# Kernel optimization log

Hardware: AMD Instinct MI355X
Metric: run time of the kernel (lower is better)

Reference implementation:

```python
import jax, jax.numpy as jnp
import numpy as np

B, T, D = 32, 1024, 1024  # batch, t_k (encoder steps), attn_sz == cell_state_sz


def setup_inputs() -> dict:
    key = jax.random.key(0)
    ks = jax.random.split(key, 7)
    scale = 1.0 / np.sqrt(D)
    return {
        "h_i": jax.random.normal(ks[0], (B, T, D), jnp.float32),
        "s_t": jax.random.normal(ks[1], (B, D), jnp.float32),
        "coverage": jax.random.uniform(ks[2], (B, T), jnp.float32),
        "W_h": jax.random.normal(ks[3], (D, D), jnp.float32) * scale,
        "W_s": jax.random.normal(ks[4], (D, D), jnp.float32) * scale,
        "b_s": jnp.zeros((D,), jnp.float32),
        "W_c": jax.random.normal(ks[5], (D,), jnp.float32) * scale,  # Dense(1 -> D) kernel
        "V_w": jax.random.normal(ks[6], (D,), jnp.float32) * scale,  # Dense(D -> 1) kernel
    }


def reference(h_i, s_t, coverage, W_h, W_s, b_s, W_c, V_w):
    # enc_features = W_h(h_i): (B, T, D)
    enc_features = jnp.einsum("btd,de->bte", h_i, W_h)
    # dec_features = W_s(s_t) broadcast over time: (B, 1, D)
    dec_features = (s_t @ W_s + b_s)[:, None, :]
    # coverage features: scalar coverage per step times (1->D) kernel
    cov_features = coverage[:, :, None] * W_c[None, None, :]
    features = enc_features + dec_features + cov_features
    # e_t = V(tanh(features)) squeezed to (B, T)
    e_t = jnp.einsum("btd,d->bt", jnp.tanh(features), V_w)
    a_t = jax.nn.softmax(e_t, axis=1)
    coverage_new = coverage + a_t
    # context = a_t @ h_i : (B, D)
    context_vector = jnp.einsum("bt,btd->bd", a_t, h_i)
    return context_vector, a_t, coverage_new
```

## Files before the change

### kernel.cpp

```cpp
#include <hip/hip_runtime.h>

#define B_ 32
#define T_ 1024
#define D_ 1024
#define M_ (B_ * T_)
#define NT_ 8
#define NT2 4
#define BM_ 128
#define BN_ 128
#define BK_ 64
#define NKT (D_ / BK_)
#define LSTR 72

#define FENCE_ALL() asm volatile("s_waitcnt vmcnt(0) lgkmcnt(0)" ::: "memory")

typedef __attribute__((ext_vector_type(8))) short short8;
typedef __attribute__((ext_vector_type(4))) float f32x4;

__device__ __forceinline__ unsigned f2bf(float f) {
    union { float f; unsigned u; } v; v.f = f;
    return (v.u + 0x7FFFu + ((v.u >> 16) & 1u)) >> 16;
}
__device__ __forceinline__ unsigned pack2(float a, float b) {
    return f2bf(a) | (f2bf(b) << 16);
}
__device__ __forceinline__ float bf2f(unsigned hi16) {
    union { unsigned u; float f; } v; v.u = hi16 << 16;
    return v.f;
}
__device__ __forceinline__ float fast_tanh(float x) {
    x = fminf(15.0f, fmaxf(-15.0f, x));
    float e = __expf(2.0f * x);
    return (e - 1.0f) * __fdividef(1.0f, e + 1.0f);
}

#define PREP_CONVH_BLKS 2048
#define PREP_CONVWT_BLKS 256
#define PREP_DEC_BLKS (B_ * 16)
__global__ __launch_bounds__(256) void prep_kernel(
    const float* __restrict__ h_i, uint4* __restrict__ h_bf4,
    const float* __restrict__ W_h, unsigned short* __restrict__ Wt,
    const float* __restrict__ s_t, const float* __restrict__ W_s,
    const float* __restrict__ b_s, float* __restrict__ dec_part)
{
    __shared__ float smem[64 * 65];
    const int bid = blockIdx.x;
    const int tid = threadIdx.x;
    if (bid < PREP_CONVH_BLKS) {
        const int idx = bid * 256 + tid;
        const int stride = PREP_CONVH_BLKS * 256;
        const int ngroups = M_ * D_ / 8;
        const float4* in4 = (const float4*)h_i;
        for (int g = idx; g < ngroups; g += stride) {
            const float4 a = in4[2 * g];
            const float4 b = in4[2 * g + 1];
            h_bf4[g] = make_uint4(pack2(a.x, a.y), pack2(a.z, a.w),
                                  pack2(b.x, b.y), pack2(b.z, b.w));
        }
    } else if (bid < PREP_CONVH_BLKS + PREP_CONVWT_BLKS) {
        const int tb = bid - PREP_CONVH_BLKS;
        float (*tile)[65] = (float (*)[65])smem;
        const int k0 = (tb & 15) * 64;
        const int n0 = (tb >> 4) * 64;
        const int tx = tid & 63, ty = tid >> 6;
#pragma unroll
        for (int r = 0; r < 16; ++r) {
            const int row = ty * 16 + r;
            tile[row][tx] = W_h[(size_t)(k0 + row) * D_ + n0 + tx];
        }
        __syncthreads();
#pragma unroll
        for (int r = 0; r < 16; ++r) {
            const int row = ty * 16 + r;
            Wt[(size_t)(n0 + row) * D_ + k0 + tx] = (unsigned short)f2bf(tile[tx][row]);
        }
    } else {
        const int db = bid - (PREP_CONVH_BLKS + PREP_CONVWT_BLKS);
        const int kc = db & 3;
        const int nc = (db >> 2) & 3;
        const int b  = db >> 4;
        const int d = nc * 256 + tid;
        const int k0 = kc * 256;
        float* s_lds = smem;
        s_lds[tid] = s_t[b * D_ + k0 + tid];
        __syncthreads();
        float acc = (kc == 0) ? b_s[d] : 0.f;
#pragma unroll 8
        for (int k = 0; k < 256; ++k) acc += s_lds[k] * W_s[(size_t)(k0 + k) * D_ + d];
        dec_part[kc * (B_ * D_) + b * D_ + d] = acc;
    }
}

__global__ __launch_bounds__(512, 2) void attn_gemm2(
    const unsigned short* __restrict__ h_bf, const unsigned short* __restrict__ wt_bf,
    const float* __restrict__ dec_part, const float* __restrict__ coverage,
    const float* __restrict__ W_c, const float* __restrict__ V_w,
    float* __restrict__ e_part)
{
    __shared__ __align__(16) unsigned short lds2[2][2][256 * 64];
    __shared__ float e_red[4][256];

    const int tid = threadIdx.x;
    const int nt2 = blockIdx.x >> 7;
    const int mt  = blockIdx.x & 127;
    const int m0 = mt * 256;
    const int n0 = nt2 * 256;
    const int bb = m0 >> 10;

    const int wave = tid >> 6;
    const int lane = tid & 63;
    const int wr = wave >> 2;
    const int wc = wave & 3;
    const int lr = lane & 15;
    const int lk = lane >> 4;

    f32x4 acc[8][4];
    const f32x4 fzero = {0.f, 0.f, 0.f, 0.f};
#pragma unroll
    for (int i = 0; i < 8; ++i)
#pragma unroll
        for (int j = 0; j < 4; ++j) acc[i][j] = fzero;

    const char* gA = (const char*)h_bf + (size_t)m0 * (D_ * 2);
    const char* gB = (const char*)wt_bf + (size_t)n0 * (D_ * 2);
    const int lrow8 = lane >> 3;
    const int scol = (((lane & 7) ^ lrow8) << 4);
    const int sw = (lr & 7) << 4;

#define GLOAD(mat, chunk, kt, buf)                                                 \
    {                                                                              \
        const int row_ = (chunk) * 8 + lrow8;                                      \
        const size_t goff_ = (size_t)row_ * (D_ * 2) + (size_t)(kt) * 128 + scol;  \
        __builtin_amdgcn_global_load_lds(                                          \
            (const __attribute__((address_space(1))) void*)(((mat) ? gB : gA) + goff_), \
            (__attribute__((address_space(3))) void*)((char*)lds2 +                \
                ((buf) * 2 + (mat)) * 32768 + (chunk) * 1024), 16, 0, 0);          \
    }
#define ST_BLO(buf, kt) { GLOAD(1, 2 * wave, kt, buf); GLOAD(1, 2 * wave + 1, kt, buf); }
#define ST_BHI(buf, kt) { GLOAD(1, 16 + 2 * wave, kt, buf); GLOAD(1, 16 + 2 * wave + 1, kt, buf); }
#define ST_AU(buf, kt, g)                                                          \
    { const int c_ = (wave < 4) ? ((g) * 4 + wave) : (16 + (g) * 4 + (wave - 4));  \
      GLOAD(0, c_, kt, buf); }

#define PH_BAR(N)                                                                  \
    asm volatile("s_waitcnt vmcnt(" #N ")" ::: "memory");                          \
    __builtin_amdgcn_s_barrier();                                                  \
    asm volatile("" ::: "memory")

#define LOADA(g)                                                                   \
    _Pragma("unroll")                                                              \
    for (int m = 0; m < 2; ++m)                                                    \
        _Pragma("unroll")                                                          \
        for (int kk = 0; kk < 2; ++kk)                                             \
            aA[m][kk] = *(const short8*)(ldsA +                                    \
                (wr * 128 + ((g) * 2 + m) * 16 + lr) * 128 +                       \
                ((kk * 64 + lk * 16) ^ sw));

#define MFMAQ(g)                                                                   \
    __builtin_amdgcn_s_setprio(1);                                                 \
    _Pragma("unroll")                                                              \
    for (int m = 0; m < 2; ++m)                                                    \
        _Pragma("unroll")                                                          \
        for (int ni = 0; ni < 4; ++ni)                                             \
            _Pragma("unroll")                                                      \
            for (int kk = 0; kk < 2; ++kk)                                         \
                acc[(g) * 2 + m][ni] = __builtin_amdgcn_mfma_f32_16x16x32_bf16(    \
                    aA[m][kk], bB[ni][kk], acc[(g) * 2 + m][ni], 0, 0, 0);         \
    __builtin_amdgcn_s_setprio(0);

    ST_BLO(0, 0); ST_BHI(0, 0);
    ST_AU(0, 0, 0); ST_AU(0, 0, 1); ST_AU(0, 0, 2); ST_AU(0, 0, 3);
    FENCE_ALL();
    __syncthreads();

    for (int kt = 0; kt < NKT; ++kt) {
        const int cur = kt & 1;
        const int nxt = cur ^ 1;
        const int ktn = (kt + 1) & (NKT - 1);
        const char* ldsA = (const char*)lds2 + (cur * 2 + 0) * 32768;
        const char* ldsB = (const char*)lds2 + (cur * 2 + 1) * 32768;

        short8 aA[2][2];
        short8 bB[4][2];

        PH_BAR(3);
#pragma unroll
        for (int ni = 0; ni < 4; ++ni)
#pragma unroll
            for (int kk = 0; kk < 2; ++kk)
                bB[ni][kk] = *(const short8*)(ldsB +
                    (wc * 64 + ni * 16 + lr) * 128 + ((kk * 64 + lk * 16) ^ sw));
        LOADA(0);
        ST_BLO(nxt, ktn);
        MFMAQ(0);

        PH_BAR(4);
        LOADA(1);
        ST_BHI(nxt, ktn);
        ST_AU(nxt, ktn, 0);
        MFMAQ(1);

        PH_BAR(5);
        LOADA(2);
        ST_AU(nxt, ktn, 1);
        ST_AU(nxt, ktn, 2);
        MFMAQ(2);

        PH_BAR(7);
        LOADA(3);
        ST_AU(nxt, ktn, 3);
        MFMAQ(3);
    }
#undef GLOAD
#undef ST_BLO
#undef ST_BHI
#undef ST_AU
#undef PH_BAR
#undef LOADA
#undef MFMAQ

    FENCE_ALL();
    __syncthreads();

    float esum[8][4];
    float covv[8][4];
#pragma unroll
    for (int mi = 0; mi < 8; ++mi)
#pragma unroll
        for (int r = 0; r < 4; ++r) {
            esum[mi][r] = 0.f;
            covv[mi][r] = coverage[m0 + wr * 128 + mi * 16 + lk * 4 + r];
        }
    const float* dp = dec_part + bb * D_;
#pragma unroll
    for (int ni = 0; ni < 4; ++ni) {
        const int n = n0 + wc * 64 + ni * 16 + lr;
        const float vw = V_w[n];
        const float dc = dp[n] + dp[B_ * D_ + n] + dp[2 * B_ * D_ + n] + dp[3 * B_ * D_ + n];
        const float wcv = W_c[n];
#pragma unroll
        for (int mi = 0; mi < 8; ++mi)
#pragma unroll
            for (int r = 0; r < 4; ++r) {
                const float f = acc[mi][ni][r] + dc + covv[mi][r] * wcv;
                esum[mi][r] += fast_tanh(f) * vw;
            }
    }
#pragma unroll
    for (int off = 1; off <= 8; off <<= 1)
#pragma unroll
        for (int mi = 0; mi < 8; ++mi)
#pragma unroll
            for (int r = 0; r < 4; ++r)
                esum[mi][r] += __shfl_xor(esum[mi][r], off, 64);

    if (lr == 0) {
#pragma unroll
        for (int mi = 0; mi < 8; ++mi)
#pragma unroll
            for (int r = 0; r < 4; ++r)
                e_red[wc][wr * 128 + mi * 16 + lk * 4 + r] = esum[mi][r];
    }
    FENCE_ALL();
    __syncthreads();
    if (tid < 256)
        e_part[(size_t)nt2 * M_ + m0 + tid] =
            e_red[0][tid] + e_red[1][tid] + e_red[2][tid] + e_red[3][tid];
}

__global__ __launch_bounds__(256, 2) void attn_gemm_kernel(
    const float* __restrict__ h_i, const float* __restrict__ W_h,
    const float* __restrict__ dec_part, const float* __restrict__ coverage,
    const float* __restrict__ W_c, const float* __restrict__ V_w,
    float* __restrict__ e_part)
{
    __shared__ __align__(16) unsigned short lA[BM_][LSTR];
    __shared__ __align__(16) unsigned short lB[BN_][LSTR];
    __shared__ float e_red[256];

    const int tid = threadIdx.x;
    const int nt = blockIdx.x >> 8;
    const int mt = blockIdx.x & 255;
    const int m0 = mt * BM_;
    const int n0 = nt * BN_;
    const int bb = m0 >> 10;

    const int wave = tid >> 6;
    const int lane = tid & 63;
    const int wr = wave >> 1, wc = wave & 1;
    const int lr = lane & 15;
    const int lk = lane >> 4;

    f32x4 acc[4][4];
    const f32x4 fzero = {0.f, 0.f, 0.f, 0.f};
#pragma unroll
    for (int i = 0; i < 4; ++i)
#pragma unroll
        for (int j = 0; j < 4; ++j) acc[i][j] = fzero;

    const int a_row = tid >> 4;
    const int a_k = (tid & 15) << 2;
    const float* hA = h_i + (size_t)m0 * D_;

    for (int k0 = 0; k0 < D_; k0 += BK_) {
#pragma unroll
        for (int p = 0; p < 8; ++p) {
            const int row = a_row + p * 16;
            const float4 v = *(const float4*)(hA + (size_t)row * D_ + (k0 + a_k));
            *(uint2*)&lA[row][a_k] = make_uint2(pack2(v.x, v.y), pack2(v.z, v.w));
        }
#pragma unroll
        for (int p = 0; p < 8; ++p) {
            const int task = tid + p * 256;
            const int n = task & 127;
            const int kg = task >> 7;
            const float* wp = W_h + (size_t)(k0 + kg * 4) * D_ + n0 + n;
            const float x0 = wp[0 * D_], x1 = wp[1 * D_], x2 = wp[2 * D_], x3 = wp[3 * D_];
            *(uint2*)&lB[n][kg * 4] = make_uint2(pack2(x0, x1), pack2(x2, x3));
        }
        __syncthreads();

        short8 af[2][4], bfr[2][4];
#pragma unroll
        for (int kk = 0; kk < 2; ++kk)
#pragma unroll
            for (int i = 0; i < 4; ++i) {
                af[kk][i]  = *(const short8*)&lA[wr * 64 + i * 16 + lr][kk * 32 + lk * 8];
                bfr[kk][i] = *(const short8*)&lB[wc * 64 + i * 16 + lr][kk * 32 + lk * 8];
            }
#pragma unroll
        for (int kk = 0; kk < 2; ++kk)
#pragma unroll
            for (int mi = 0; mi < 4; ++mi)
#pragma unroll
                for (int ni = 0; ni < 4; ++ni)
                    acc[mi][ni] = __builtin_amdgcn_mfma_f32_16x16x32_bf16(
                        af[kk][mi], bfr[kk][ni], acc[mi][ni], 0, 0, 0);
        __syncthreads();
    }

    float esum[4][4];
    float covv[4][4];
#pragma unroll
    for (int mi = 0; mi < 4; ++mi)
#pragma unroll
        for (int r = 0; r < 4; ++r) {
            esum[mi][r] = 0.f;
            covv[mi][r] = coverage[m0 + wr * 64 + mi * 16 + lk * 4 + r];
        }
    const float* dp = dec_part + bb * D_;
#pragma unroll
    for (int ni = 0; ni < 4; ++ni) {
        const int n = n0 + wc * 64 + ni * 16 + lr;
        const float vw = V_w[n];
        const float dc = dp[n] + dp[B_ * D_ + n] + dp[2 * B_ * D_ + n] + dp[3 * B_ * D_ + n];
        const float wcv = W_c[n];
#pragma unroll
        for (int mi = 0; mi < 4; ++mi)
#pragma unroll
            for (int r = 0; r < 4; ++r) {
                const float f = acc[mi][ni][r] + dc + covv[mi][r] * wcv;
                esum[mi][r] += fast_tanh(f) * vw;
            }
    }
#pragma unroll
    for (int off = 1; off <= 8; off <<= 1)
#pragma unroll
        for (int mi = 0; mi < 4; ++mi)
#pragma unroll
            for (int r = 0; r < 4; ++r)
                esum[mi][r] += __shfl_xor(esum[mi][r], off, 64);

    if (lr == 0) {
#pragma unroll
        for (int mi = 0; mi < 4; ++mi)
#pragma unroll
            for (int r = 0; r < 4; ++r)
                e_red[wc * 128 + wr * 64 + mi * 16 + lk * 4 + r] = esum[mi][r];
    }
    __syncthreads();
    if (tid < 128)
        e_part[(size_t)nt * M_ + m0 + tid] = e_red[tid] + e_red[128 + tid];
}

__global__ __launch_bounds__(256) void softmax_kernel(
    const float* __restrict__ e_part, const float* __restrict__ coverage,
    float* __restrict__ a_out, float* __restrict__ cov_out,
    float* __restrict__ a_ws, int nparts)
{
    const int b = blockIdx.x;
    const int tid = threadIdx.x;
    __shared__ float redmx[4], redsum[4];
    float e[4];
#pragma unroll
    for (int j = 0; j < 4; ++j) {
        const int t = tid + j * 256;
        float s = 0.f;
        for (int p = 0; p < nparts; ++p) s += e_part[(size_t)p * M_ + b * T_ + t];
        e[j] = s;
    }
    float mx = fmaxf(fmaxf(e[0], e[1]), fmaxf(e[2], e[3]));
#pragma unroll
    for (int off = 32; off > 0; off >>= 1) mx = fmaxf(mx, __shfl_xor(mx, off, 64));
    if ((tid & 63) == 0) redmx[tid >> 6] = mx;
    __syncthreads();
    mx = fmaxf(fmaxf(redmx[0], redmx[1]), fmaxf(redmx[2], redmx[3]));
    float p4[4];
    float ps = 0.f;
#pragma unroll
    for (int j = 0; j < 4; ++j) { p4[j] = __expf(e[j] - mx); ps += p4[j]; }
#pragma unroll
    for (int off = 32; off > 0; off >>= 1) ps += __shfl_xor(ps, off, 64);
    if ((tid & 63) == 0) redsum[tid >> 6] = ps;
    __syncthreads();
    ps = redsum[0] + redsum[1] + redsum[2] + redsum[3];
    const float inv = __fdividef(1.f, ps);
#pragma unroll
    for (int j = 0; j < 4; ++j) {
        const int idx = b * T_ + tid + j * 256;
        const float a = p4[j] * inv;
        a_out[idx] = a;
        a_ws[idx] = a;
        cov_out[idx] = coverage[idx] + a;
    }
}

__global__ __launch_bounds__(256) void ctx_part_bf(
    const unsigned short* __restrict__ h_bf, const float* __restrict__ a_t,
    float* __restrict__ ctx_part)
{
    const int bid = blockIdx.x;
    const int b = bid >> 3;
    const int dc = (bid >> 2) & 1;
    const int tc = bid & 3;
    const int tid = threadIdx.x;
    const int d0 = dc * 512 + tid * 2;
    __shared__ float a_lds[256];
    a_lds[tid] = a_t[b * T_ + tc * 256 + tid];
    __syncthreads();
    const unsigned short* hp = h_bf + ((size_t)(b * T_ + tc * 256)) * D_ + d0;
    float acc0 = 0.f, acc1 = 0.f;
#pragma unroll 8
    for (int t = 0; t < 256; ++t) {
        const unsigned v = *(const unsigned*)(hp + (size_t)t * D_);
        const float a = a_lds[t];
        acc0 += a * bf2f(v & 0xFFFFu);
        acc1 += a * bf2f(v >> 16);
    }
    *(float2*)(ctx_part + tc * (B_ * D_) + b * D_ + d0) = make_float2(acc0, acc1);
}

__global__ __launch_bounds__(256) void ctx_part_f32(
    const float* __restrict__ h_i, const float* __restrict__ a_t,
    float* __restrict__ ctx_part)
{
    const int bid = blockIdx.x;
    const int b = bid >> 4;
    const int dc = (bid >> 2) & 3;
    const int tc = bid & 3;
    const int tid = threadIdx.x;
    const int d = dc * 256 + tid;
    __shared__ float a_lds[256];
    a_lds[tid] = a_t[b * T_ + tc * 256 + tid];
    __syncthreads();
    const float* hp = h_i + ((size_t)(b * T_ + tc * 256)) * D_ + d;
    float acc = 0.f;
#pragma unroll 8
    for (int t = 0; t < 256; ++t) acc += a_lds[t] * hp[(size_t)t * D_];
    ctx_part[tc * (B_ * D_) + b * D_ + d] = acc;
}

__global__ __launch_bounds__(256) void dec_kernel(
    const float* __restrict__ s_t, const float* __restrict__ W_s,
    const float* __restrict__ b_s, float* __restrict__ dec_part)
{
    const int bid = blockIdx.x;
    const int kc = bid & 3;
    const int nc = (bid >> 2) & 3;
    const int b  = bid >> 4;
    const int d = nc * 256 + threadIdx.x;
    const int k0 = kc * 256;
    __shared__ float s_lds[256];
    s_lds[threadIdx.x] = s_t[b * D_ + k0 + threadIdx.x];
    __syncthreads();
    float acc = (kc == 0) ? b_s[d] : 0.f;
#pragma unroll 8
    for (int k = 0; k < 256; ++k) acc += s_lds[k] * W_s[(size_t)(k0 + k) * D_ + d];
    dec_part[kc * (B_ * D_) + b * D_ + d] = acc;
}

__global__ __launch_bounds__(256) void ctx_reduce_kernel(
    const float* __restrict__ ctx_part, float* __restrict__ out)
{
    const int i = blockIdx.x * 256 + threadIdx.x;
    out[i] = ctx_part[i] + ctx_part[B_ * D_ + i] + ctx_part[2 * B_ * D_ + i] +
             ctx_part[3 * B_ * D_ + i];
}

extern "C" void kernel_launch(void* const* d_in, const int* in_sizes, int n_in,
                              void* d_out, int out_size, void* d_ws, size_t ws_size,
                              hipStream_t stream)
{
    (void)in_sizes; (void)n_in; (void)out_size;
    const float* h_i      = (const float*)d_in[0];
    const float* s_t      = (const float*)d_in[1];
    const float* coverage = (const float*)d_in[2];
    const float* W_h      = (const float*)d_in[3];
    const float* W_s      = (const float*)d_in[4];
    const float* b_s      = (const float*)d_in[5];
    const float* W_c      = (const float*)d_in[6];
    const float* V_w      = (const float*)d_in[7];

    float* out     = (float*)d_out;
    float* ctx_out = out;
    float* a_out   = out + B_ * T_;
    float* cov_out = out + 2 * B_ * T_;

    float* ws       = (float*)d_ws;
    float* dec_part = ws;
    float* e_part   = dec_part + 4 * B_ * D_;
    float* ctx_part = e_part + NT_ * M_;
    float* a_ws     = ctx_part + 4 * B_ * D_;
    const size_t f32_count = 8 * (size_t)B_ * D_ + (size_t)NT_ * M_ + (size_t)B_ * T_;
    unsigned short* h_bf  = (unsigned short*)(ws + f32_count);
    unsigned short* wt_bf = h_bf + (size_t)M_ * D_;
    const size_t need = f32_count * 4 + ((size_t)M_ * D_ + (size_t)D_ * D_) * 2;

    if (ws_size >= need) {
        prep_kernel<<<PREP_CONVH_BLKS + PREP_CONVWT_BLKS + PREP_DEC_BLKS, 256, 0, stream>>>(
            h_i, (uint4*)h_bf, W_h, wt_bf, s_t, W_s, b_s, dec_part);
        attn_gemm2<<<NT2 * (M_ / 256), 512, 0, stream>>>(h_bf, wt_bf, dec_part,
                                                         coverage, W_c, V_w, e_part);
        softmax_kernel<<<B_, 256, 0, stream>>>(e_part, coverage, a_out, cov_out, a_ws, NT2);
        ctx_part_bf<<<B_ * 8, 256, 0, stream>>>(h_bf, a_ws, ctx_part);
    } else {
        dec_kernel<<<B_ * 16, 256, 0, stream>>>(s_t, W_s, b_s, dec_part);
        attn_gemm_kernel<<<NT_ * (M_ / BM_), 256, 0, stream>>>(h_i, W_h, dec_part,
                                                               coverage, W_c, V_w, e_part);
        softmax_kernel<<<B_, 256, 0, stream>>>(e_part, coverage, a_out, cov_out, a_ws, NT_);
        ctx_part_f32<<<B_ * 16, 256, 0, stream>>>(h_i, a_ws, ctx_part);
    }
    ctx_reduce_kernel<<<(B_ * D_) / 256, 256, 0, stream>>>(ctx_part, ctx_out);
}
```

Before: 149.7 us.

## Restructure GEMM phase synchronization with barriers around each MFMA block

Each phase of the GEMM main loop previously waited on vmcnt and then hit one workgroup barrier before reading LDS. Now it waits only on vmcnt, issues the LDS fragment reads and the next global-to-LDS prefetches, then runs the MFMA block between two s_barriers, with an lgkmcnt(0) wait and sched_barrier fences. The aim is to keep waves in lockstep around MFMA bursts and to let LDS reads and prefetch issue overlap better. In exchange it doubles the barriers per phase. Some LDS reads now happen before a barrier that guarantees other waves' async loads have landed, which risks a data race.

```diff
diff --git a/kernel.cpp b/kernel.cpp
--- a/kernel.cpp
+++ b/kernel.cpp
@@ -142,10 +142,10 @@
     { const int c_ = (wave < 4) ? ((g) * 4 + wave) : (16 + (g) * 4 + (wave - 4));  \
       GLOAD(0, c_, kt, buf); }
 
-#define PH_BAR(N)                                                                  \
-    asm volatile("s_waitcnt vmcnt(" #N ")" ::: "memory");                          \
-    __builtin_amdgcn_s_barrier();                                                  \
-    asm volatile("" ::: "memory")
+#define VM_WAIT(N) asm volatile("s_waitcnt vmcnt(" #N ")" ::: "memory")
+#define LGKM0()                                                                    \
+    asm volatile("s_waitcnt lgkmcnt(0)" ::: "memory");                             \
+    __builtin_amdgcn_sched_barrier(0)
 
 #define LOADA(g)                                                                   \
     _Pragma("unroll")                                                              \
@@ -168,6 +168,13 @@
                     aA[m][kk], bB[ni][kk], acc[(g) * 2 + m][ni], 0, 0, 0);         \
     __builtin_amdgcn_s_setprio(0);
 
+#define PH_COMPUTE(g)                                                              \
+    __builtin_amdgcn_sched_barrier(0);                                             \
+    __builtin_amdgcn_s_barrier();                                                  \
+    LGKM0();                                                                       \
+    MFMAQ(g);                                                                      \
+    __builtin_amdgcn_s_barrier()
+
     ST_BLO(0, 0); ST_BHI(0, 0);
     ST_AU(0, 0, 0); ST_AU(0, 0, 1); ST_AU(0, 0, 2); ST_AU(0, 0, 3);
     FENCE_ALL();
@@ -183,7 +190,7 @@
         short8 aA[2][2];
         short8 bB[4][2];
 
-        PH_BAR(3);
+        VM_WAIT(3);
 #pragma unroll
         for (int ni = 0; ni < 4; ++ni)
 #pragma unroll
@@ -192,32 +199,34 @@
                     (wc * 64 + ni * 16 + lr) * 128 + ((kk * 64 + lk * 16) ^ sw));
         LOADA(0);
         ST_BLO(nxt, ktn);
-        MFMAQ(0);
-
-        PH_BAR(4);
+        PH_COMPUTE(0);
+
+        VM_WAIT(4);
         LOADA(1);
         ST_BHI(nxt, ktn);
         ST_AU(nxt, ktn, 0);
-        MFMAQ(1);
-
-        PH_BAR(5);
+        PH_COMPUTE(1);
+
+        VM_WAIT(5);
         LOADA(2);
         ST_AU(nxt, ktn, 1);
         ST_AU(nxt, ktn, 2);
-        MFMAQ(2);
-
-        PH_BAR(7);
+        PH_COMPUTE(2);
+
+        VM_WAIT(7);
         LOADA(3);
         ST_AU(nxt, ktn, 3);
-        MFMAQ(3);
+        PH_COMPUTE(3);
     }
 #undef GLOAD
 #undef ST_BLO
 #undef ST_BHI
 #undef ST_AU
-#undef PH_BAR
+#undef VM_WAIT
+#undef LGKM0
 #undef LOADA
 #undef MFMAQ
+#undef PH_COMPUTE
 
     FENCE_ALL();
     __syncthreads();
```

After: 153.1 us. 1.02x slower.

## Fuse softmax, context accumulation and reduction into one post kernel

Applied to the files above, without the earlier changes.

Replaces the softmax, ctx_part_bf and ctx_reduce launches on the bf16 path with a single post_kernel. Each of its 256 blocks recomputes the softmax for its batch row, keeps the attention weights in LDS, and reduces its 128-column context slice in shared memory. This removes two kernel launches and the global round-trips for a_ws and ctx_part. The cost is that softmax is computed eight times per batch row, and the context loop now reads strided 128-column slices across four time quarters per block.

```diff
diff --git a/kernel.cpp b/kernel.cpp
--- a/kernel.cpp
+++ b/kernel.cpp
@@ -268,6 +268,79 @@
             e_red[0][tid] + e_red[1][tid] + e_red[2][tid] + e_red[3][tid];
 }
 
+__global__ __launch_bounds__(256) void post_kernel(
+    const float* __restrict__ e_part, const float* __restrict__ coverage,
+    const unsigned short* __restrict__ h_bf,
+    float* __restrict__ a_out, float* __restrict__ cov_out,
+    float* __restrict__ ctx_out)
+{
+    const int bid = blockIdx.x;
+    const int b = bid >> 3;
+    const int s = bid & 7;
+    const int tid = threadIdx.x;
+    __shared__ float a_lds[T_];
+    __shared__ float redmx[4], redsum[4];
+    __shared__ float cred[4][128];
+
+    float e[4];
+#pragma unroll
+    for (int j = 0; j < 4; ++j) {
+        const int t = tid + j * 256;
+        float ssum = 0.f;
+#pragma unroll
+        for (int p = 0; p < NT2; ++p) ssum += e_part[(size_t)p * M_ + b * T_ + t];
+        e[j] = ssum;
+    }
+    float mx = fmaxf(fmaxf(e[0], e[1]), fmaxf(e[2], e[3]));
+#pragma unroll
+    for (int off = 32; off > 0; off >>= 1) mx = fmaxf(mx, __shfl_xor(mx, off, 64));
+    if ((tid & 63) == 0) redmx[tid >> 6] = mx;
+    __syncthreads();
+    mx = fmaxf(fmaxf(redmx[0], redmx[1]), fmaxf(redmx[2], redmx[3]));
+    float p4[4];
+    float ps = 0.f;
+#pragma unroll
+    for (int j = 0; j < 4; ++j) { p4[j] = __expf(e[j] - mx); ps += p4[j]; }
+#pragma unroll
+    for (int off = 32; off > 0; off >>= 1) ps += __shfl_xor(ps, off, 64);
+    if ((tid & 63) == 0) redsum[tid >> 6] = ps;
+    __syncthreads();
+    ps = redsum[0] + redsum[1] + redsum[2] + redsum[3];
+    const float inv = __fdividef(1.f, ps);
+#pragma unroll
+    for (int j = 0; j < 4; ++j) {
+        const int t = tid + j * 256;
+        const float a = p4[j] * inv;
+        a_lds[t] = a;
+        if (s == 0) {
+            const int idx = b * T_ + t;
+            a_out[idx] = a;
+            cov_out[idx] = coverage[idx] + a;
+        }
+    }
+    __syncthreads();
+
+    const int dp = (tid & 63) * 2;
+    const int q  = tid >> 6;
+    const int d0 = s * 128 + dp;
+    const unsigned short* hp = h_bf + ((size_t)(b * T_ + q * 256)) * D_ + d0;
+    const float* al = a_lds + q * 256;
+    float acc0 = 0.f, acc1 = 0.f;
+#pragma unroll 8
+    for (int t = 0; t < 256; ++t) {
+        const unsigned v = *(const unsigned*)(hp + (size_t)t * D_);
+        const float a = al[t];
+        acc0 += a * bf2f(v & 0xFFFFu);
+        acc1 += a * bf2f(v >> 16);
+    }
+    cred[q][dp] = acc0;
+    cred[q][dp + 1] = acc1;
+    __syncthreads();
+    if (tid < 128)
+        ctx_out[b * D_ + s * 128 + tid] =
+            cred[0][tid] + cred[1][tid] + cred[2][tid] + cred[3][tid];
+}
+
 __global__ __launch_bounds__(256, 2) void attn_gemm_kernel(
     const float* __restrict__ h_i, const float* __restrict__ W_h,
     const float* __restrict__ dec_part, const float* __restrict__ coverage,
@@ -395,9 +468,9 @@
 #pragma unroll
     for (int j = 0; j < 4; ++j) {
         const int t = tid + j * 256;
-        float s = 0.f;
-        for (int p = 0; p < nparts; ++p) s += e_part[(size_t)p * M_ + b * T_ + t];
-        e[j] = s;
+        float ssum = 0.f;
+        for (int p = 0; p < nparts; ++p) ssum += e_part[(size_t)p * M_ + b * T_ + t];
+        e[j] = ssum;
     }
     float mx = fmaxf(fmaxf(e[0], e[1]), fmaxf(e[2], e[3]));
 #pragma unroll
@@ -423,31 +496,6 @@
         a_ws[idx] = a;
         cov_out[idx] = coverage[idx] + a;
     }
-}
-
-__global__ __launch_bounds__(256) void ctx_part_bf(
-    const unsigned short* __restrict__ h_bf, const float* __restrict__ a_t,
-    float* __restrict__ ctx_part)
-{
-    const int bid = blockIdx.x;
-    const int b = bid >> 3;
-    const int dc = (bid >> 2) & 1;
-    const int tc = bid & 3;
-    const int tid = threadIdx.x;
-    const int d0 = dc * 512 + tid * 2;
-    __shared__ float a_lds[256];
-    a_lds[tid] = a_t[b * T_ + tc * 256 + tid];
-    __syncthreads();
-    const unsigned short* hp = h_bf + ((size_t)(b * T_ + tc * 256)) * D_ + d0;
-    float acc0 = 0.f, acc1 = 0.f;
-#pragma unroll 8
-    for (int t = 0; t < 256; ++t) {
-        const unsigned v = *(const unsigned*)(hp + (size_t)t * D_);
-        const float a = a_lds[t];
-        acc0 += a * bf2f(v & 0xFFFFu);
-        acc1 += a * bf2f(v >> 16);
-    }
-    *(float2*)(ctx_part + tc * (B_ * D_) + b * D_ + d0) = make_float2(acc0, acc1);
 }
 
 __global__ __launch_bounds__(256) void ctx_part_f32(
@@ -531,14 +579,14 @@
             h_i, (uint4*)h_bf, W_h, wt_bf, s_t, W_s, b_s, dec_part);
         attn_gemm2<<<NT2 * (M_ / 256), 512, 0, stream>>>(h_bf, wt_bf, dec_part,
                                                          coverage, W_c, V_w, e_part);
-        softmax_kernel<<<B_, 256, 0, stream>>>(e_part, coverage, a_out, cov_out, a_ws, NT2);
-        ctx_part_bf<<<B_ * 8, 256, 0, stream>>>(h_bf, a_ws, ctx_part);
+        post_kernel<<<B_ * 8, 256, 0, stream>>>(e_part, coverage, h_bf,
+                                                a_out, cov_out, ctx_out);
     } else {
         dec_kernel<<<B_ * 16, 256, 0, stream>>>(s_t, W_s, b_s, dec_part);
         attn_gemm_kernel<<<NT_ * (M_ / BM_), 256, 0, stream>>>(h_i, W_h, dec_part,
                                                                coverage, W_c, V_w, e_part);
         softmax_kernel<<<B_, 256, 0, stream>>>(e_part, coverage, a_out, cov_out, a_ws, NT_);
         ctx_part_f32<<<B_ * 16, 256, 0, stream>>>(h_i, a_ws, ctx_part);
-    }
-    ctx_reduce_kernel<<<(B_ * D_) / 256, 256, 0, stream>>>(ctx_part, ctx_out);
-}
+        ctx_reduce_kernel<<<(B_ * D_) / 256, 256, 0, stream>>>(ctx_part, ctx_out);
+    }
+}
```

Result: faster. 135.5 us (-9.5%).
